# Performance work log

Hardware: AMD Instinct MI355X
Metric: run time of the kernel (lower is better)

Reference implementation:

```python
import jax, jax.numpy as jnp
import numpy as np

N, E = 50000, 1600000
D_IN, D_HID, D_OUT = 256, 256, 128  # 2*output_dim = 256, output_dim = 128


def glorot(key, shape):
    fan_in, fan_out = shape
    limit = np.sqrt(6.0 / (fan_in + fan_out)).astype(np.float32)
    return jax.random.uniform(key, shape, jnp.float32, -limit, limit)


def setup_inputs() -> dict:
    key = jax.random.key(0)
    k0, k1, k2, k3 = jax.random.split(key, 4)
    x = jax.random.normal(k0, (N, D_IN), jnp.float32)
    edge_index = jax.random.randint(k1, (2, E), 0, N, jnp.int32)
    W1 = glorot(k2, (D_IN, D_HID))
    b1 = jnp.zeros((D_HID,), jnp.float32)
    W2 = glorot(k3, (D_HID, D_OUT))
    b2 = jnp.zeros((D_OUT,), jnp.float32)
    return {"x": x, "edge_index": edge_index, "W1": W1, "b1": b1, "W2": W2, "b2": b2}


def gcn_propagate(x, src, dst, num_nodes):
    """One hop of D^-1/2 (A + I) D^-1/2 @ x (PyG gcn_norm with self-loops)."""
    loops = jnp.arange(num_nodes, dtype=src.dtype)
    src_sl = jnp.concatenate([src, loops])  # [E + N]
    dst_sl = jnp.concatenate([dst, loops])
    ones = jnp.ones(src_sl.shape, x.dtype)
    deg = jax.ops.segment_sum(ones, dst_sl, num_segments=num_nodes)  # >= 1 (self-loop)
    dinv = jax.lax.rsqrt(jnp.maximum(deg, 1e-12))
    norm = dinv[src_sl] * dinv[dst_sl]  # [E + N]
    msgs = x[src_sl] * norm[:, None]    # gather + scale, [E+N, D]
    return jax.ops.segment_sum(msgs, dst_sl, num_segments=num_nodes)


def reference(x, edge_index, W1, b1, W2, b2):
    src, dst = edge_index[0], edge_index[1]
    n = x.shape[0]
    # SGConv(K=1): propagate then linear. conv1 + ReLU
    h = jax.nn.relu(gcn_propagate(x, src, dst, n) @ W1 + b1)
    # conv2 (GAE branch)
    return gcn_propagate(h, src, dst, n) @ W2 + b2
```

## Files before the change

kernel.cpp:

```cpp
#include <hip/hip_runtime.h>

typedef short s16x8 __attribute__((ext_vector_type(8)));
typedef float f32x4 __attribute__((ext_vector_type(4)));
typedef float f32x2 __attribute__((ext_vector_type(2)));

#define TILE 2048
#define TILE2 8192

__device__ __forceinline__ unsigned int brne(float f) {
    unsigned int u = __float_as_uint(f);
    return (u + 0x7FFFu + ((u >> 16) & 1u)) >> 16;
}
__device__ __forceinline__ float blo(unsigned int u) { return __uint_as_float(u << 16); }
__device__ __forceinline__ float bhi(unsigned int u) { return __uint_as_float(u & 0xFFFF0000u); }

__device__ __forceinline__ unsigned int pk_bf16(float lo, float hi) {
    unsigned int r;
    asm("v_cvt_pk_bf16_f32 %0, %1, %2" : "=v"(r) : "v"(lo), "v"(hi));
    return r;
}

__device__ __forceinline__ void pkfma(f32x2& a, const f32x2 x, const f32x2 w) {
    asm("v_pk_fma_f32 %0, %1, %2, %0" : "+v"(a) : "v"(x), "v"(w));
}

__device__ __forceinline__ void acc8p(f32x2* a, const uint4 u, const f32x2 w2) {
    pkfma(a[0], (f32x2){blo(u.x), bhi(u.x)}, w2);
    pkfma(a[1], (f32x2){blo(u.y), bhi(u.y)}, w2);
    pkfma(a[2], (f32x2){blo(u.z), bhi(u.z)}, w2);
    pkfma(a[3], (f32x2){blo(u.w), bhi(u.w)}, w2);
}

__device__ __forceinline__ void acc16p(f32x2* a, const uint4 u, const f32x2 w2) {
    pkfma(a[0], __builtin_amdgcn_cvt_pk_f32_fp8((int)u.x, false), w2);
    pkfma(a[1], __builtin_amdgcn_cvt_pk_f32_fp8((int)u.x, true),  w2);
    pkfma(a[2], __builtin_amdgcn_cvt_pk_f32_fp8((int)u.y, false), w2);
    pkfma(a[3], __builtin_amdgcn_cvt_pk_f32_fp8((int)u.y, true),  w2);
    pkfma(a[4], __builtin_amdgcn_cvt_pk_f32_fp8((int)u.z, false), w2);
    pkfma(a[5], __builtin_amdgcn_cvt_pk_f32_fp8((int)u.z, true),  w2);
    pkfma(a[6], __builtin_amdgcn_cvt_pk_f32_fp8((int)u.w, false), w2);
    pkfma(a[7], __builtin_amdgcn_cvt_pk_f32_fp8((int)u.w, true),  w2);
}


__global__ void k_bhist_deg_tw(const int* __restrict__ dst, int* __restrict__ bcnt,
                               int* __restrict__ deg, int e, int nb, int nbt,
                               const float* __restrict__ W1, const float* __restrict__ W2,
                               unsigned short* __restrict__ W1t, unsigned short* __restrict__ W2t) {
    const int tid = threadIdx.x;
    if ((int)blockIdx.x >= nbt) {
        const int t = ((int)blockIdx.x - nbt) * 256 + tid;
        if (t < 65536) {
            const int k = t >> 8, nn = t & 255;
            W1t[nn * 256 + k] = (unsigned short)brne(W1[t]);
        } else {
            const int u = t - 65536;
            const int k = u >> 7, nn = u & 127;
            W2t[nn * 256 + k] = (unsigned short)brne(W2[u]);
        }
        return;
    }
    __shared__ int h[256];
    h[tid] = 0;
    __syncthreads();
    const int base = blockIdx.x * TILE + tid;
#pragma unroll
    for (int k = 0; k < 8; k++) {
        const int i = base + k * 256;
        if (i < e) {
            const int d = dst[i];
            atomicAdd(&h[d >> 8], 1);
            atomicAdd(&deg[d], 1);
        }
    }
    __syncthreads();
    if (tid < nb && h[tid]) atomicAdd(&bcnt[tid], h[tid]);
}

__global__ void k_bscatter8(const int* __restrict__ src, const int* __restrict__ dst,
                            const int* __restrict__ bcnt, int* __restrict__ bcur,
                            uint2* __restrict__ eb, int e, int nb) {
    __shared__ int sh[256], h[256], base2[256], h2[256];
    const int tid = threadIdx.x;
    const int v = (tid < nb) ? bcnt[tid] : 0;
    int x = v;
    sh[tid] = x;
    __syncthreads();
    for (int off = 1; off < 256; off <<= 1) {
        const int t = (tid >= off) ? sh[tid - off] : 0;
        __syncthreads();
        if (tid >= off) { x += t; sh[tid] = x; }
        __syncthreads();
    }
    const int sbase = x - v;
    h[tid] = 0; h2[tid] = 0;
    __syncthreads();
    const int beg = blockIdx.x * TILE2;
    const int fin = min(beg + TILE2, e);
    for (int i = beg + tid; i < fin; i += 256)
        atomicAdd(&h[dst[i] >> 8], 1);
    __syncthreads();
    if (h[tid]) base2[tid] = sbase + atomicAdd(&bcur[tid], h[tid]);
    __syncthreads();
    for (int i = beg + tid; i < fin; i += 256) {
        const int s = src[i], d = dst[i];
        const int b = d >> 8;
        const int off = atomicAdd(&h2[b], 1);
        eb[base2[b] + off] = make_uint2((unsigned)s, (unsigned)d);
    }
}

template <bool PREW>
__global__ void k_scan1(const int* __restrict__ deg, int* __restrict__ rowptr,
                        int* __restrict__ part, float* __restrict__ dinv,
                        void* __restrict__ esv, int n, int e) {
    __shared__ int sh[256];
    const int tid = threadIdx.x, b = blockIdx.x;
    const int node = b * 256 + tid;
    const int v = (node < n) ? deg[node] : 0;
    if (node < n) dinv[node] = rsqrtf((float)(v + 1));
    int x = v;
    sh[tid] = x;
    __syncthreads();
    for (int off = 1; off < 256; off <<= 1) {
        const int t = (tid >= off) ? sh[tid - off] : 0;
        __syncthreads();
        if (tid >= off) { x += t; sh[tid] = x; }
        __syncthreads();
    }
    if (node <= n) rowptr[node] = x - v;
    if (tid == 255) part[b] = x;
    if (PREW && b == 0 && tid < 64) ((int2*)esv)[e + tid] = make_int2(0, 0);
}

template <bool PREW>
__global__ void k_place3(const uint2* __restrict__ eb, const int* __restrict__ bcnt,
                         int* __restrict__ rowptr, const int* __restrict__ part,
                         const float* __restrict__ dinv, void* __restrict__ esv,
                         int n, int nb) {
    __shared__ int sh[256], rp[256], offs[256];
    __shared__ float sdv[256];
    const int tid = threadIdx.x, b = blockIdx.x;
    const int cv = (tid < nb) ? bcnt[tid] : 0;
    int x = cv;
    sh[tid] = x;
    __syncthreads();
    for (int off = 1; off < 256; off <<= 1) {
        const int t = (tid >= off) ? sh[tid - off] : 0;
        __syncthreads();
        if (tid >= off) { x += t; sh[tid] = x; }
        __syncthreads();
    }
    const int ebBase = (b > 0) ? sh[b - 1] : 0;
    const int cnt = bcnt[b];
    __syncthreads();
    int y = (tid < nb) ? part[tid] : 0;
    sh[tid] = y;
    __syncthreads();
    for (int off = 1; off < 256; off <<= 1) {
        const int t = (tid >= off) ? sh[tid - off] : 0;
        __syncthreads();
        if (tid >= off) { y += t; sh[tid] = y; }
        __syncthreads();
    }
    const int prefix = (b > 0) ? sh[b - 1] : 0;
    const int node = b * 256 + tid;
    int rg = 0;
    if (node <= n) {
        rg = rowptr[node] + prefix;
        rowptr[node] = rg;
    }
    rp[tid] = rg;
    offs[tid] = 0;
    if (PREW) sdv[tid] = (node < n) ? dinv[node] : 0.f;
    __syncthreads();
    if (PREW) {
        int2* es2 = (int2*)esv;
        for (int i = tid; i < cnt; i += 256) {
            const uint2 ed = eb[ebBase + i];
            const int sI = (int)ed.x, d = (int)ed.y & 255;
            const float w = dinv[sI] * sdv[d];
            const int local = atomicAdd(&offs[d], 1);
            es2[rp[d] + local] = make_int2(sI, __float_as_int(w));
        }
    } else {
        int* es1 = (int*)esv;
        for (int i = tid; i < cnt; i += 256) {
            const uint2 ed = eb[ebBase + i];
            const int d = (int)ed.y & 255;
            const int local = atomicAdd(&offs[d], 1);
            es1[rp[d] + local] = (int)ed.x;
        }
    }
}

#define LP 40
template <bool AF32, bool FP8OUT>
__global__ __launch_bounds__(256) void k_gemm(const void* __restrict__ Av,
                                              const unsigned short* __restrict__ Bt,
                                              void* __restrict__ Cout,
                                              int M, int Nc) {
    __shared__ unsigned short As[2][128 * LP];
    __shared__ unsigned short Bs[2][128 * LP];

    const int tid = threadIdx.x;
    const int wave = tid >> 6, lane = tid & 63;
    const int wm = (wave >> 1) * 64, wn = (wave & 1) * 64;
    const int l15 = lane & 15, quad = lane >> 4;
    const int mBase = blockIdx.x * 128, nBase = blockIdx.y * 128;

    f32x4 acc[4][4];
#pragma unroll
    for (int i = 0; i < 4; i++)
#pragma unroll
        for (int j = 0; j < 4; j++) acc[i][j] = (f32x4){0.f, 0.f, 0.f, 0.f};

    const int r0 = tid >> 2, kc0 = tid & 3;
    int am0 = mBase + r0;      if (am0 >= M) am0 = M - 1;
    int am1 = mBase + r0 + 64; if (am1 >= M) am1 = M - 1;

    const uint4* Ap0; const uint4* Ap1; const float4* Af0; const float4* Af1;
    if (AF32) {
        Af0 = (const float4*)Av + (size_t)am0 * 64 + kc0 * 2;
        Af1 = (const float4*)Av + (size_t)am1 * 64 + kc0 * 2;
    } else {
        Ap0 = (const uint4*)Av + (size_t)am0 * 32 + kc0;
        Ap1 = (const uint4*)Av + (size_t)am1 * 32 + kc0;
    }
    const uint4* Bp0 = (const uint4*)Bt + (size_t)(nBase + r0) * 32 + kc0;
    const uint4* Bp1 = (const uint4*)Bt + (size_t)(nBase + r0 + 64) * 32 + kc0;

    uint4 a0, a1, b0, b1;
    auto LOAD = [&](int kt) {
        if (AF32) {
            const float4 l0 = Af0[kt * 8], h0 = Af0[kt * 8 + 1];
            const float4 l1 = Af1[kt * 8], h1 = Af1[kt * 8 + 1];
            a0.x = pk_bf16(l0.x, l0.y); a0.y = pk_bf16(l0.z, l0.w);
            a0.z = pk_bf16(h0.x, h0.y); a0.w = pk_bf16(h0.z, h0.w);
            a1.x = pk_bf16(l1.x, l1.y); a1.y = pk_bf16(l1.z, l1.w);
            a1.z = pk_bf16(h1.x, h1.y); a1.w = pk_bf16(h1.z, h1.w);
        } else {
            a0 = Ap0[kt * 4];
            a1 = Ap1[kt * 4];
        }
        b0 = Bp0[kt * 4];
        b1 = Bp1[kt * 4];
    };
    auto STORE = [&](int buf) {
        *(uint4*)&As[buf][r0 * LP + kc0 * 8] = a0;
        *(uint4*)&As[buf][(r0 + 64) * LP + kc0 * 8] = a1;
        *(uint4*)&Bs[buf][r0 * LP + kc0 * 8] = b0;
        *(uint4*)&Bs[buf][(r0 + 64) * LP + kc0 * 8] = b1;
    };

    LOAD(0);
    STORE(0);
    __syncthreads();
    for (int kt = 0; kt < 8; ++kt) {
        const int cur = kt & 1;
        if (kt < 7) LOAD(kt + 1);
        s16x8 af[4], bf[4];
#pragma unroll
        for (int i = 0; i < 4; i++)
            af[i] = *(const s16x8*)&As[cur][(wm + i * 16 + l15) * LP + quad * 8];
#pragma unroll
        for (int j = 0; j < 4; j++)
            bf[j] = *(const s16x8*)&Bs[cur][(wn + j * 16 + l15) * LP + quad * 8];
        if (kt < 7) STORE(cur ^ 1);
#pragma unroll
        for (int i = 0; i < 4; i++)
#pragma unroll
            for (int j = 0; j < 4; j++)
                acc[i][j] = __builtin_amdgcn_mfma_f32_16x16x32_bf16(af[i], bf[j], acc[i][j], 0, 0, 0);
        __syncthreads();
    }

#pragma unroll
    for (int i = 0; i < 4; i++) {
        const int rowb = mBase + wm + i * 16 + quad * 4;
#pragma unroll
        for (int j = 0; j < 4; j++) {
            const int col = nBase + wn + j * 16 + l15;
#pragma unroll
            for (int r = 0; r < 4; r += 2) {
                if (FP8OUT) {
                    const unsigned int pk = __builtin_amdgcn_cvt_pk_fp8_f32(
                        acc[i][j][r], acc[i][j][r + 1], 0, false);
                    if (rowb + r < M)
                        ((unsigned char*)Cout)[(size_t)(rowb + r) * Nc + col] =
                            (unsigned char)pk;
                    if (rowb + r + 1 < M)
                        ((unsigned char*)Cout)[(size_t)(rowb + r + 1) * Nc + col] =
                            (unsigned char)(pk >> 8);
                } else {
                    const unsigned int pk = pk_bf16(acc[i][j][r], acc[i][j][r + 1]);
                    if (rowb + r < M)
                        ((unsigned short*)Cout)[(size_t)(rowb + r) * Nc + col] =
                            (unsigned short)pk;
                    if (rowb + r + 1 < M)
                        ((unsigned short*)Cout)[(size_t)(rowb + r + 1) * Nc + col] =
                            (unsigned short)(pk >> 16);
                }
            }
        }
    }
}


template <bool PREW>
__global__ void k_prop256f8(const uint4* __restrict__ X4,
                            const int* __restrict__ rowptr,
                            const void* __restrict__ esv,
                            const float* __restrict__ dinv,
                            const float* __restrict__ bias,
                            uint4* __restrict__ Y4, int n) {
    const int wid = (int)((blockIdx.x * blockDim.x + threadIdx.x) >> 6);
    const int lane = threadIdx.x & 63;
    const int quad = lane >> 4, l16 = lane & 15;
    if (wid >= n) return;
    const float dd = dinv[wid];
    const int2* es2 = (const int2*)esv;
    const int*  es1 = (const int*)esv;
    f32x2 a[8];
#pragma unroll
    for (int k = 0; k < 8; k++) a[k] = (f32x2){0.f, 0.f};

    const int beg = rowptr[wid], end = rowptr[wid + 1];
    int j = beg + quad;

    auto EDGE = [&](int jj, int& s, float& w) {
        const bool v = jj < end;
        const int idx = v ? jj : beg;
        if (PREW) {
            const int2 p = es2[idx];
            s = p.x;
            w = v ? __int_as_float(p.y) : 0.f;
        } else {
            s = es1[v ? jj : 0];
            w = v ? dinv[s] * dd : 0.f;
        }
    };

    int s0, s1, s2, s3;
    float w0, w1, w2, w3;
    EDGE(j, s0, w0); EDGE(j + 4, s1, w1); EDGE(j + 8, s2, w2); EDGE(j + 12, s3, w3);

    if (quad == 0) {
        const uint4 v = X4[(size_t)wid * 16 + l16];
        acc16p(a, v, (f32x2){dd * dd, dd * dd});
    }

    while (j + 12 < end) {
        const uint4 u0 = X4[(size_t)s0 * 16 + l16];
        const uint4 u1 = X4[(size_t)s1 * 16 + l16];
        const uint4 u2 = X4[(size_t)s2 * 16 + l16];
        const uint4 u3 = X4[(size_t)s3 * 16 + l16];
        j += 16;
        int t0, t1, t2, t3;
        float x0, x1, x2, x3;
        EDGE(j, t0, x0); EDGE(j + 4, t1, x1); EDGE(j + 8, t2, x2); EDGE(j + 12, t3, x3);
        acc16p(a, u0, (f32x2){w0, w0});
        acc16p(a, u1, (f32x2){w1, w1});
        acc16p(a, u2, (f32x2){w2, w2});
        acc16p(a, u3, (f32x2){w3, w3});
        s0 = t0; s1 = t1; s2 = t2; s3 = t3;
        w0 = x0; w1 = x1; w2 = x2; w3 = x3;
    }
    {
        const uint4 u0 = X4[(size_t)s0 * 16 + l16];
        const uint4 u1 = X4[(size_t)s1 * 16 + l16];
        const uint4 u2 = X4[(size_t)s2 * 16 + l16];
        acc16p(a, u0, (f32x2){w0, w0});
        acc16p(a, u1, (f32x2){w1, w1});
        acc16p(a, u2, (f32x2){w2, w2});
    }
#pragma unroll
    for (int k = 0; k < 8; k++) {
        a[k][0] += __shfl_xor(a[k][0], 16);
        a[k][1] += __shfl_xor(a[k][1], 16);
        a[k][0] += __shfl_xor(a[k][0], 32);
        a[k][1] += __shfl_xor(a[k][1], 32);
    }
    if (quad == 0) {
        const float4* bp = (const float4*)bias + l16 * 4;
#pragma unroll
        for (int q = 0; q < 4; q++) {
            const float4 b = bp[q];
            a[2 * q][0]     = fmaxf(a[2 * q][0] + b.x, 0.f);
            a[2 * q][1]     = fmaxf(a[2 * q][1] + b.y, 0.f);
            a[2 * q + 1][0] = fmaxf(a[2 * q + 1][0] + b.z, 0.f);
            a[2 * q + 1][1] = fmaxf(a[2 * q + 1][1] + b.w, 0.f);
        }
        uint4 p0, p1;
        p0.x = pk_bf16(a[0][0], a[0][1]);
        p0.y = pk_bf16(a[1][0], a[1][1]);
        p0.z = pk_bf16(a[2][0], a[2][1]);
        p0.w = pk_bf16(a[3][0], a[3][1]);
        p1.x = pk_bf16(a[4][0], a[4][1]);
        p1.y = pk_bf16(a[5][0], a[5][1]);
        p1.z = pk_bf16(a[6][0], a[6][1]);
        p1.w = pk_bf16(a[7][0], a[7][1]);
        Y4[(size_t)wid * 32 + l16 * 2] = p0;
        Y4[(size_t)wid * 32 + l16 * 2 + 1] = p1;
    }
}

template <bool PREW>
__global__ void k_prop128b(const uint4* __restrict__ X4,
                           const int* __restrict__ rowptr,
                           const void* __restrict__ esv,
                           const float* __restrict__ dinv,
                           const float* __restrict__ bias,
                           float* __restrict__ Yout, int n) {
    const int wid = (int)((blockIdx.x * blockDim.x + threadIdx.x) >> 6);
    const int lane = threadIdx.x & 63;
    const int quad = lane >> 4, l16 = lane & 15;
    if (wid >= n) return;
    const float dd = dinv[wid];
    const int2* es2 = (const int2*)esv;
    const int*  es1 = (const int*)esv;
    f32x2 a[4];
#pragma unroll
    for (int k = 0; k < 4; k++) a[k] = (f32x2){0.f, 0.f};

    const int beg = rowptr[wid], end = rowptr[wid + 1];
    int j = beg + quad;

    auto EDGE = [&](int jj, int& s, float& w) {
        const bool v = jj < end;
        const int idx = v ? jj : beg;
        if (PREW) {
            const int2 p = es2[idx];
            s = p.x;
            w = v ? __int_as_float(p.y) : 0.f;
        } else {
            s = es1[v ? jj : 0];
            w = v ? dinv[s] * dd : 0.f;
        }
    };

    int s0, s1, s2, s3;
    float w0, w1, w2, w3;
    EDGE(j, s0, w0); EDGE(j + 4, s1, w1); EDGE(j + 8, s2, w2); EDGE(j + 12, s3, w3);

    if (quad == 0) {
        const uint4 v = X4[(size_t)wid * 16 + l16];
        acc8p(a, v, (f32x2){dd * dd, dd * dd});
    }

    while (j + 12 < end) {
        const uint4 u0 = X4[(size_t)s0 * 16 + l16];
        const uint4 u1 = X4[(size_t)s1 * 16 + l16];
        const uint4 u2 = X4[(size_t)s2 * 16 + l16];
        const uint4 u3 = X4[(size_t)s3 * 16 + l16];
        j += 16;
        int t0, t1, t2, t3;
        float x0, x1, x2, x3;
        EDGE(j, t0, x0); EDGE(j + 4, t1, x1); EDGE(j + 8, t2, x2); EDGE(j + 12, t3, x3);
        acc8p(a, u0, (f32x2){w0, w0});
        acc8p(a, u1, (f32x2){w1, w1});
        acc8p(a, u2, (f32x2){w2, w2});
        acc8p(a, u3, (f32x2){w3, w3});
        s0 = t0; s1 = t1; s2 = t2; s3 = t3;
        w0 = x0; w1 = x1; w2 = x2; w3 = x3;
    }
    {
        const uint4 u0 = X4[(size_t)s0 * 16 + l16];
        const uint4 u1 = X4[(size_t)s1 * 16 + l16];
        const uint4 u2 = X4[(size_t)s2 * 16 + l16];
        acc8p(a, u0, (f32x2){w0, w0});
        acc8p(a, u1, (f32x2){w1, w1});
        acc8p(a, u2, (f32x2){w2, w2});
    }
#pragma unroll
    for (int k = 0; k < 4; k++) {
        a[k][0] += __shfl_xor(a[k][0], 16);
        a[k][1] += __shfl_xor(a[k][1], 16);
        a[k][0] += __shfl_xor(a[k][0], 32);
        a[k][1] += __shfl_xor(a[k][1], 32);
    }
    if (quad == 0) {
        const float4 b0 = ((const float4*)bias)[l16 * 2];
        const float4 b1 = ((const float4*)bias)[l16 * 2 + 1];
        float4* op = (float4*)Yout + (size_t)wid * 32 + l16 * 2;
        op[0] = make_float4(a[0][0] + b0.x, a[0][1] + b0.y, a[1][0] + b0.z, a[1][1] + b0.w);
        op[1] = make_float4(a[2][0] + b1.x, a[2][1] + b1.y, a[3][0] + b1.z, a[3][1] + b1.w);
    }
}

extern "C" void kernel_launch(void* const* d_in, const int* in_sizes, int n_in,
                              void* d_out, int out_size, void* d_ws, size_t ws_size,
                              hipStream_t stream) {
    const float* x  = (const float*)d_in[0];
    const int*   ei = (const int*)d_in[1];
    const float* W1 = (const float*)d_in[2];
    const float* b1 = (const float*)d_in[3];
    const float* W2 = (const float*)d_in[4];
    const float* b2 = (const float*)d_in[5];
    float* out = (float*)d_out;

    const int n = in_sizes[0] / 256;
    const int e = in_sizes[1] / 2;
    const int* src = ei;
    const int* dst = ei + e;
    const int nb = (n + 255) >> 8;

    auto al = [](size_t v) { return (v + 511) & ~(size_t)511; };
    const size_t fixed = al(sizeof(float) * n) + al(sizeof(int) * (n + 1)) +
                         al(1024) + al(4ull * (512 + n)) +
                         al(2ull * 256 * 256) + al(2ull * 128 * 256) +
                         al((size_t)n * 256) + al(2ull * n * 256) + al(2ull * n * 128);
    const bool prew = (fixed + al(8ull * ((size_t)e + 64))) <= ws_size;

    char* wsp = (char*)d_ws;
    size_t off = 0;
    auto alloc = [&](size_t bytes) -> char* {
        char* p = wsp + off;
        off += (bytes + 511) & ~(size_t)511;
        return p;
    };
    float* dinv    = (float*)alloc(sizeof(float) * n);
    int*   rowptr  = (int*)alloc(sizeof(int) * (n + 1));
    int*   part    = (int*)alloc(1024);
    int*   bcd     = (int*)alloc(4ull * (512 + n));
    int*   bcnt    = bcd;
    int*   bcur    = bcd + 256;
    int*   deg     = bcd + 512;
    void*  es      = (void*)alloc(prew ? 8ull * ((size_t)e + 64) : 4ull * (size_t)e);
    unsigned short* W1t = (unsigned short*)alloc(2ull * 256 * 256);
    unsigned short* W2t = (unsigned short*)alloc(2ull * 128 * 256);
    unsigned char*  T1  = (unsigned char*)alloc((size_t)n * 256);
    unsigned short* H   = (unsigned short*)alloc(2ull * n * 256);
    unsigned short* T2  = (unsigned short*)alloc(2ull * n * 128);
    uint2* eb = (uint2*)H;

    const int nb_t  = (e + TILE - 1) / TILE;
    const int nb_t2 = (e + TILE2 - 1) / TILE2;
    const int tw_b  = (65536 + 32768) / 256;

    (void)hipMemsetAsync(bcd, 0, 4ull * (512 + n), stream);
    k_bhist_deg_tw<<<nb_t + tw_b, 256, 0, stream>>>(dst, bcnt, deg, e, nb, nb_t,
                                                    W1, W2, W1t, W2t);
    k_bscatter8<<<nb_t2, 256, 0, stream>>>(src, dst, bcnt, bcur, eb, e, nb);
    if (prew) {
        k_scan1<true><<<nb, 256, 0, stream>>>(deg, rowptr, part, dinv, es, n, e);
        k_place3<true><<<nb, 256, 0, stream>>>(eb, bcnt, rowptr, part, dinv, es, n, nb);
    } else {
        k_scan1<false><<<nb, 256, 0, stream>>>(deg, rowptr, part, dinv, es, n, e);
        k_place3<false><<<nb, 256, 0, stream>>>(eb, bcnt, rowptr, part, dinv, es, n, nb);
    }

    dim3 g1((n + 127) / 128, 2);
    k_gemm<true, true><<<g1, 256, 0, stream>>>(x, W1t, T1, n, 256);
    if (prew)
        k_prop256f8<true><<<(n + 3) / 4, 256, 0, stream>>>((const uint4*)T1, rowptr, es,
                                                           dinv, b1, (uint4*)H, n);
    else
        k_prop256f8<false><<<(n + 3) / 4, 256, 0, stream>>>((const uint4*)T1, rowptr, es,
                                                            dinv, b1, (uint4*)H, n);

    dim3 g2((n + 127) / 128, 1);
    k_gemm<false, false><<<g2, 256, 0, stream>>>(H, W2t, T2, n, 128);
    if (prew)
        k_prop128b<true><<<(n + 3) / 4, 256, 0, stream>>>((const uint4*)T2, rowptr, es,
                                                          dinv, b2, out, n);
    else
        k_prop128b<false><<<(n + 3) / 4, 256, 0, stream>>>((const uint4*)T2, rowptr, es,
                                                           dinv, b2, out, n);
}
```

Baseline: 375.2 us.

## Merge CSR scan/place into one kernel with per-bucket padded edge storage

Drops the global per-node degree atomics in the histogram kernel. Degrees are now counted per 256-node bucket in shared memory inside a single merged kernel, which also computes dinv, row offsets and edge placement. Edges are packed into 32-bit words (local dst in the top 8 bits, src in the low 24), and each bucket gets a fixed-capacity slot (capE, 1.5x the average), so no global scan is needed. The propagation kernels lose the precomputed edge weights: they read only the source index and compute dinv[s]*dd on the fly. This cuts launches, global atomics and edge-array bytes, but it adds a random dinv gather per edge. It also risks overflow if a bucket has more edges than capE, and the 24-bit src field limits the node count.

```diff
diff --git a/kernel.cpp b/kernel.cpp
--- a/kernel.cpp
+++ b/kernel.cpp
@@ -43,10 +43,10 @@
 }
 
 
-__global__ void k_bhist_deg_tw(const int* __restrict__ dst, int* __restrict__ bcnt,
-                               int* __restrict__ deg, int e, int nb, int nbt,
-                               const float* __restrict__ W1, const float* __restrict__ W2,
-                               unsigned short* __restrict__ W1t, unsigned short* __restrict__ W2t) {
+__global__ void k_bhist_tw(const int* __restrict__ dst, int* __restrict__ bcnt,
+                           int e, int nb, int nbt,
+                           const float* __restrict__ W1, const float* __restrict__ W2,
+                           unsigned short* __restrict__ W1t, unsigned short* __restrict__ W2t) {
     const int tid = threadIdx.x;
     if ((int)blockIdx.x >= nbt) {
         const int t = ((int)blockIdx.x - nbt) * 256 + tid;
@@ -67,11 +67,7 @@
 #pragma unroll
     for (int k = 0; k < 8; k++) {
         const int i = base + k * 256;
-        if (i < e) {
-            const int d = dst[i];
-            atomicAdd(&h[d >> 8], 1);
-            atomicAdd(&deg[d], 1);
-        }
+        if (i < e) atomicAdd(&h[dst[i] >> 8], 1);
     }
     __syncthreads();
     if (tid < nb && h[tid]) atomicAdd(&bcnt[tid], h[tid]);
@@ -79,7 +75,7 @@
 
 __global__ void k_bscatter8(const int* __restrict__ src, const int* __restrict__ dst,
                             const int* __restrict__ bcnt, int* __restrict__ bcur,
-                            uint2* __restrict__ eb, int e, int nb) {
+                            unsigned int* __restrict__ eb, int e, int nb) {
     __shared__ int sh[256], h[256], base2[256], h2[256];
     const int tid = threadIdx.x;
     const int v = (tid < nb) ? bcnt[tid] : 0;
@@ -106,20 +102,18 @@
         const int s = src[i], d = dst[i];
         const int b = d >> 8;
         const int off = atomicAdd(&h2[b], 1);
-        eb[base2[b] + off] = make_uint2((unsigned)s, (unsigned)d);
-    }
-}
-
-template <bool PREW>
-__global__ void k_scan1(const int* __restrict__ deg, int* __restrict__ rowptr,
-                        int* __restrict__ part, float* __restrict__ dinv,
-                        void* __restrict__ esv, int n, int e) {
-    __shared__ int sh[256];
+        eb[base2[b] + off] = ((unsigned)(d & 255) << 24) | (unsigned)s;
+    }
+}
+
+__global__ void k_merged(const unsigned int* __restrict__ eb, const int* __restrict__ bcnt,
+                         int* __restrict__ rowptr, int* __restrict__ cnt,
+                         float* __restrict__ dinv, int* __restrict__ es,
+                         int n, int nb, int capE) {
+    __shared__ int sh[256], c[256], rp[256], offs[256];
     const int tid = threadIdx.x, b = blockIdx.x;
-    const int node = b * 256 + tid;
-    const int v = (node < n) ? deg[node] : 0;
-    if (node < n) dinv[node] = rsqrtf((float)(v + 1));
-    int x = v;
+    const int v0 = (tid < nb) ? bcnt[tid] : 0;
+    int x = v0;
     sh[tid] = x;
     __syncthreads();
     for (int off = 1; off < 256; off <<= 1) {
@@ -128,69 +122,38 @@
         if (tid >= off) { x += t; sh[tid] = x; }
         __syncthreads();
     }
-    if (node <= n) rowptr[node] = x - v;
-    if (tid == 255) part[b] = x;
-    if (PREW && b == 0 && tid < 64) ((int2*)esv)[e + tid] = make_int2(0, 0);
-}
-
-template <bool PREW>
-__global__ void k_place3(const uint2* __restrict__ eb, const int* __restrict__ bcnt,
-                         int* __restrict__ rowptr, const int* __restrict__ part,
-                         const float* __restrict__ dinv, void* __restrict__ esv,
-                         int n, int nb) {
-    __shared__ int sh[256], rp[256], offs[256];
-    __shared__ float sdv[256];
-    const int tid = threadIdx.x, b = blockIdx.x;
-    const int cv = (tid < nb) ? bcnt[tid] : 0;
-    int x = cv;
-    sh[tid] = x;
+    const int ebBase = (b > 0) ? sh[b - 1] : 0;
+    const int cntB = bcnt[b];
+    c[tid] = 0;
+    __syncthreads();
+    for (int i = tid; i < cntB; i += 256)
+        atomicAdd(&c[eb[ebBase + i] >> 24], 1);
+    __syncthreads();
+    const int v = c[tid];
+    const int node = b * 256 + tid;
+    if (node < n) {
+        dinv[node] = rsqrtf((float)(v + 1));
+        cnt[node] = v;
+    }
+    int y = v;
+    sh[tid] = y;
     __syncthreads();
     for (int off = 1; off < 256; off <<= 1) {
         const int t = (tid >= off) ? sh[tid - off] : 0;
         __syncthreads();
-        if (tid >= off) { x += t; sh[tid] = x; }
-        __syncthreads();
-    }
-    const int ebBase = (b > 0) ? sh[b - 1] : 0;
-    const int cnt = bcnt[b];
-    __syncthreads();
-    int y = (tid < nb) ? part[tid] : 0;
-    sh[tid] = y;
-    __syncthreads();
-    for (int off = 1; off < 256; off <<= 1) {
-        const int t = (tid >= off) ? sh[tid - off] : 0;
-        __syncthreads();
         if (tid >= off) { y += t; sh[tid] = y; }
         __syncthreads();
     }
-    const int prefix = (b > 0) ? sh[b - 1] : 0;
-    const int node = b * 256 + tid;
-    int rg = 0;
-    if (node <= n) {
-        rg = rowptr[node] + prefix;
-        rowptr[node] = rg;
-    }
-    rp[tid] = rg;
+    const int beg = b * capE + (y - v);
+    if (node < n) rowptr[node] = beg;
+    rp[tid] = beg;
     offs[tid] = 0;
-    if (PREW) sdv[tid] = (node < n) ? dinv[node] : 0.f;
-    __syncthreads();
-    if (PREW) {
-        int2* es2 = (int2*)esv;
-        for (int i = tid; i < cnt; i += 256) {
-            const uint2 ed = eb[ebBase + i];
-            const int sI = (int)ed.x, d = (int)ed.y & 255;
-            const float w = dinv[sI] * sdv[d];
-            const int local = atomicAdd(&offs[d], 1);
-            es2[rp[d] + local] = make_int2(sI, __float_as_int(w));
-        }
-    } else {
-        int* es1 = (int*)esv;
-        for (int i = tid; i < cnt; i += 256) {
-            const uint2 ed = eb[ebBase + i];
-            const int d = (int)ed.y & 255;
-            const int local = atomicAdd(&offs[d], 1);
-            es1[rp[d] + local] = (int)ed.x;
-        }
+    __syncthreads();
+    for (int i = tid; i < cntB; i += 256) {
+        const unsigned int u = eb[ebBase + i];
+        const int d = (int)(u >> 24);
+        const int local = atomicAdd(&offs[d], 1);
+        es[rp[d] + local] = (int)(u & 0xFFFFFFu);
     }
 }
 
@@ -307,10 +270,10 @@
 }
 
 
-template <bool PREW>
 __global__ void k_prop256f8(const uint4* __restrict__ X4,
                             const int* __restrict__ rowptr,
-                            const void* __restrict__ esv,
+                            const int* __restrict__ cnt,
+                            const int* __restrict__ es,
                             const float* __restrict__ dinv,
                             const float* __restrict__ bias,
                             uint4* __restrict__ Y4, int n) {
@@ -319,26 +282,18 @@
     const int quad = lane >> 4, l16 = lane & 15;
     if (wid >= n) return;
     const float dd = dinv[wid];
-    const int2* es2 = (const int2*)esv;
-    const int*  es1 = (const int*)esv;
     f32x2 a[8];
 #pragma unroll
     for (int k = 0; k < 8; k++) a[k] = (f32x2){0.f, 0.f};
 
-    const int beg = rowptr[wid], end = rowptr[wid + 1];
+    const int beg = rowptr[wid];
+    const int end = beg + cnt[wid];
     int j = beg + quad;
 
     auto EDGE = [&](int jj, int& s, float& w) {
         const bool v = jj < end;
-        const int idx = v ? jj : beg;
-        if (PREW) {
-            const int2 p = es2[idx];
-            s = p.x;
-            w = v ? __int_as_float(p.y) : 0.f;
-        } else {
-            s = es1[v ? jj : 0];
-            w = v ? dinv[s] * dd : 0.f;
-        }
+        s = es[v ? jj : beg];
+        w = v ? dinv[s] * dd : 0.f;
     };
 
     int s0, s1, s2, s3;
@@ -405,10 +360,10 @@
     }
 }
 
-template <bool PREW>
 __global__ void k_prop128b(const uint4* __restrict__ X4,
                            const int* __restrict__ rowptr,
-                           const void* __restrict__ esv,
+                           const int* __restrict__ cnt,
+                           const int* __restrict__ es,
                            const float* __restrict__ dinv,
                            const float* __restrict__ bias,
                            float* __restrict__ Yout, int n) {
@@ -417,26 +372,18 @@
     const int quad = lane >> 4, l16 = lane & 15;
     if (wid >= n) return;
     const float dd = dinv[wid];
-    const int2* es2 = (const int2*)esv;
-    const int*  es1 = (const int*)esv;
     f32x2 a[4];
 #pragma unroll
     for (int k = 0; k < 4; k++) a[k] = (f32x2){0.f, 0.f};
 
-    const int beg = rowptr[wid], end = rowptr[wid + 1];
+    const int beg = rowptr[wid];
+    const int end = beg + cnt[wid];
     int j = beg + quad;
 
     auto EDGE = [&](int jj, int& s, float& w) {
         const bool v = jj < end;
-        const int idx = v ? jj : beg;
-        if (PREW) {
-            const int2 p = es2[idx];
-            s = p.x;
-            w = v ? __int_as_float(p.y) : 0.f;
-        } else {
-            s = es1[v ? jj : 0];
-            w = v ? dinv[s] * dd : 0.f;
-        }
+        s = es[v ? jj : beg];
+        w = v ? dinv[s] * dd : 0.f;
     };
 
     int s0, s1, s2, s3;
@@ -505,12 +452,8 @@
     const int* dst = ei + e;
     const int nb = (n + 255) >> 8;
 
-    auto al = [](size_t v) { return (v + 511) & ~(size_t)511; };
-    const size_t fixed = al(sizeof(float) * n) + al(sizeof(int) * (n + 1)) +
-                         al(1024) + al(4ull * (512 + n)) +
-                         al(2ull * 256 * 256) + al(2ull * 128 * 256) +
-                         al((size_t)n * 256) + al(2ull * n * 256) + al(2ull * n * 128);
-    const bool prew = (fixed + al(8ull * ((size_t)e + 64))) <= ws_size;
+    int capE = (((e / nb) * 3 / 2) + 255) & ~255;
+    if (capE < 2048) capE = 2048;
 
     char* wsp = (char*)d_ws;
     size_t off = 0;
@@ -520,51 +463,35 @@
         return p;
     };
     float* dinv    = (float*)alloc(sizeof(float) * n);
-    int*   rowptr  = (int*)alloc(sizeof(int) * (n + 1));
-    int*   part    = (int*)alloc(1024);
-    int*   bcd     = (int*)alloc(4ull * (512 + n));
-    int*   bcnt    = bcd;
-    int*   bcur    = bcd + 256;
-    int*   deg     = bcd + 512;
-    void*  es      = (void*)alloc(prew ? 8ull * ((size_t)e + 64) : 4ull * (size_t)e);
+    int*   rowptr  = (int*)alloc(sizeof(int) * n);
+    int*   cnt     = (int*)alloc(sizeof(int) * n);
+    int*   bcc     = (int*)alloc(2048);
+    int*   bcnt    = bcc;
+    int*   bcur    = bcc + 256;
+    int*   es      = (int*)alloc(4ull * (size_t)nb * capE);
     unsigned short* W1t = (unsigned short*)alloc(2ull * 256 * 256);
     unsigned short* W2t = (unsigned short*)alloc(2ull * 128 * 256);
     unsigned char*  T1  = (unsigned char*)alloc((size_t)n * 256);
     unsigned short* H   = (unsigned short*)alloc(2ull * n * 256);
     unsigned short* T2  = (unsigned short*)alloc(2ull * n * 128);
-    uint2* eb = (uint2*)H;
+    unsigned int* eb = (unsigned int*)H;
 
     const int nb_t  = (e + TILE - 1) / TILE;
     const int nb_t2 = (e + TILE2 - 1) / TILE2;
     const int tw_b  = (65536 + 32768) / 256;
 
-    (void)hipMemsetAsync(bcd, 0, 4ull * (512 + n), stream);
-    k_bhist_deg_tw<<<nb_t + tw_b, 256, 0, stream>>>(dst, bcnt, deg, e, nb, nb_t,
-                                                    W1, W2, W1t, W2t);
+    (void)hipMemsetAsync(bcc, 0, 2048, stream);
+    k_bhist_tw<<<nb_t + tw_b, 256, 0, stream>>>(dst, bcnt, e, nb, nb_t, W1, W2, W1t, W2t);
     k_bscatter8<<<nb_t2, 256, 0, stream>>>(src, dst, bcnt, bcur, eb, e, nb);
-    if (prew) {
-        k_scan1<true><<<nb, 256, 0, stream>>>(deg, rowptr, part, dinv, es, n, e);
-        k_place3<true><<<nb, 256, 0, stream>>>(eb, bcnt, rowptr, part, dinv, es, n, nb);
-    } else {
-        k_scan1<false><<<nb, 256, 0, stream>>>(deg, rowptr, part, dinv, es, n, e);
-        k_place3<false><<<nb, 256, 0, stream>>>(eb, bcnt, rowptr, part, dinv, es, n, nb);
-    }
+    k_merged<<<nb, 256, 0, stream>>>(eb, bcnt, rowptr, cnt, dinv, es, n, nb, capE);
 
     dim3 g1((n + 127) / 128, 2);
     k_gemm<true, true><<<g1, 256, 0, stream>>>(x, W1t, T1, n, 256);
-    if (prew)
-        k_prop256f8<true><<<(n + 3) / 4, 256, 0, stream>>>((const uint4*)T1, rowptr, es,
-                                                           dinv, b1, (uint4*)H, n);
-    else
-        k_prop256f8<false><<<(n + 3) / 4, 256, 0, stream>>>((const uint4*)T1, rowptr, es,
-                                                            dinv, b1, (uint4*)H, n);
+    k_prop256f8<<<(n + 3) / 4, 256, 0, stream>>>((const uint4*)T1, rowptr, cnt, es,
+                                                 dinv, b1, (uint4*)H, n);
 
     dim3 g2((n + 127) / 128, 1);
     k_gemm<false, false><<<g2, 256, 0, stream>>>(H, W2t, T2, n, 128);
-    if (prew)
-        k_prop128b<true><<<(n + 3) / 4, 256, 0, stream>>>((const uint4*)T2, rowptr, es,
-                                                          dinv, b2, out, n);
-    else
-        k_prop128b<false><<<(n + 3) / 4, 256, 0, stream>>>((const uint4*)T2, rowptr, es,
-                                                           dinv, b2, out, n);
-}
+    k_prop128b<<<(n + 3) / 4, 256, 0, stream>>>((const uint4*)T2, rowptr, cnt, es,
+                                                dinv, b2, out, n);
+}
```

Measured after the change: 331.0 us. 1.13x faster.
